# Kernel tuning notes

Hardware: AMD Instinct MI355X
Metric: run time of the kernel (lower is better)

Reference implementation:

```python
import math
import jax, jax.numpy as jnp
import numpy as np

B, S, D, H = 2, 2048, 1024, 16
DH = D // H


def setup_inputs() -> dict:
    key = jax.random.key(0)
    ks = jax.random.split(key, 6)
    scale = 1.0 / math.sqrt(D)  # xavier-ish scale for stability
    inp = {
        "query": jax.random.normal(ks[0], (B, S, D), jnp.float32),
        "mask": jax.random.randint(ks[1], (B, S, S), 0, 2) > 0,
        "Wq": jax.random.normal(ks[2], (D, D), jnp.float32) * scale,
        "bq": jnp.zeros((D,), jnp.float32),
        "Wk": jax.random.normal(ks[3], (D, D), jnp.float32) * scale,
        "bk": jnp.zeros((D,), jnp.float32),
        "Wv": jax.random.normal(ks[4], (D, D), jnp.float32) * scale,
        "bv": jnp.zeros((D,), jnp.float32),
        "Wo": jax.random.normal(ks[5], (D, D), jnp.float32) * scale,
        "bo": jnp.zeros((D,), jnp.float32),
    }
    return inp


def reference(query, mask, Wq, bq, Wk, bk, Wv, bv, Wo, bo):
    # self-attention: memory = query
    def shape(x):  # [B,S,D] -> [B,H,S,DH]
        return x.reshape(B, S, H, DH).transpose(0, 2, 1, 3)

    q = shape(query @ Wq.T + bq) / math.sqrt(DH)
    k = shape(query @ Wk.T + bk)
    v = shape(query @ Wv.T + bv)
    scores = jnp.einsum("bhqd,bhkd->bhqk", q, k)
    scores = jnp.where(mask[:, None, :, :], jnp.float32(-1e18), scores)
    attn = jax.nn.softmax(scores, axis=-1)
    # dropout is identity in eval mode
    ctx = jnp.einsum("bhqk,bhkd->bhqd", attn, v)
    ctx = ctx.transpose(0, 2, 1, 3).reshape(B, S, D)
    return ctx @ Wo.T + bo
```

## Files before the change

### kernel.cpp

```cpp
#include <hip/hip_runtime.h>

#define B_ 2
#define S_ 2048
#define D_ 1024
#define H_ 16
#define DH_ 64

typedef float f32x4 __attribute__((ext_vector_type(4)));
typedef short s16x8 __attribute__((ext_vector_type(8)));
typedef __bf16 bf16x8 __attribute__((ext_vector_type(8)));
typedef unsigned int uint;

template <typename T>
static __device__ auto mfma_sel(T a, T b, f32x4 c, int)
    -> decltype(__builtin_amdgcn_mfma_f32_16x16x32_bf16(a, b, c, 0, 0, 0)) {
  return __builtin_amdgcn_mfma_f32_16x16x32_bf16(a, b, c, 0, 0, 0);
}
template <typename T>
static __device__ f32x4 mfma_sel(T a, T b, f32x4 c, long) {
  return __builtin_amdgcn_mfma_f32_16x16x32_bf16(
      __builtin_bit_cast(bf16x8, a), __builtin_bit_cast(bf16x8, b), c, 0, 0, 0);
}
static __device__ __forceinline__ f32x4 mfma_bf16(s16x8 a, s16x8 b, f32x4 c) {
  return mfma_sel(a, b, c, 0);
}

static __device__ __forceinline__ short f2bf(float f) {
  unsigned u = __float_as_uint(f);
  u += 0x7fffu + ((u >> 16) & 1u);
  return (short)(u >> 16);
}

static __device__ __forceinline__ short f2bf_rn(float f) {
  return __builtin_bit_cast(short, (__bf16)f);
}

static __device__ __forceinline__ void async16(const short* g, short* l) {
  __builtin_amdgcn_global_load_lds(
      (const __attribute__((address_space(1))) unsigned int*)g,
      (__attribute__((address_space(3))) unsigned int*)l, 16, 0, 0);
}

__global__ void detect_mask_kernel(const uint* __restrict__ m,
                                   int* __restrict__ flag) {
  int lane = threadIdx.x;
  bool gt1 = false, notf = false;
  for (int i = 0; i < 16; ++i) {
    uint v = m[lane * 16 + i];
    if (v > 1u) gt1 = true;
    if (v != 0u && v != 0x3F800000u) notf = true;
  }
  unsigned long long b1 = __ballot(gt1);
  unsigned long long b2 = __ballot(notf);
  if (lane == 0) {
    int f;
    if (b1 == 0ull) f = 1;
    else if (b2 == 0ull) f = 2;
    else f = 0;
    *flag = f;
  }
}

__global__ __launch_bounds__(256) void build_bitmask_kernel(
    const void* __restrict__ mask, const int* __restrict__ flag,
    uint* __restrict__ bmT) {
  int w = blockIdx.x * 256 + threadIdx.x;
  int b = w >> 17;
  int rem = w & 131071;
  int q = rem >> 6;
  int kt = rem & 63;
  int mty = *flag;
  uint bits = 0;
  if (mty == 0) {
    const uint* p = (const uint*)((const unsigned char*)mask +
                                  ((size_t)b * S_ + q) * S_ + (size_t)kt * 32);
#pragma unroll
    for (int i = 0; i < 8; ++i) {
      uint v = p[i];
#pragma unroll
      for (int j = 0; j < 4; ++j)
        if ((v >> (8 * j)) & 0xffu) bits |= 1u << (i * 4 + j);
    }
  } else {
    const uint* p = (const uint*)mask + ((size_t)b * S_ + q) * S_ + kt * 32;
#pragma unroll
    for (int i = 0; i < 32; ++i)
      if (p[i]) bits |= 1u << i;
  }
  bmT[((size_t)b * (S_ / 32) + kt) * S_ + q] = bits;
}

__global__ __launch_bounds__(256) void convert_kernel(
    const float* __restrict__ q, const float* __restrict__ wq,
    const float* __restrict__ wk, const float* __restrict__ wv,
    short* __restrict__ qbf, short* __restrict__ wqkv) {
  int bid = blockIdx.x;
  int t = threadIdx.x;
  const float* src;
  short* dst;
  int rowbase, seg;
  if (bid < 2048)      { src = q;  dst = qbf;  rowbase = bid * 2;          seg = -1; }
  else if (bid < 2560) { src = wq; dst = wqkv; rowbase = (bid - 2048) * 2; seg = 0; }
  else if (bid < 3072) { src = wk; dst = wqkv; rowbase = (bid - 2560) * 2; seg = 1; }
  else                 { src = wv; dst = wqkv; rowbase = (bid - 3072) * 2; seg = 2; }
  int rl = rowbase + (t >> 7);
  int k = (t & 127) * 8;
  const float* s8 = src + (size_t)rl * 1024 + k;
  f32x4 a = *(const f32x4*)s8;
  f32x4 b = *(const f32x4*)(s8 + 4);
  s16x8 r;
  r[0] = f2bf(a[0]); r[1] = f2bf(a[1]); r[2] = f2bf(a[2]); r[3] = f2bf(a[3]);
  r[4] = f2bf(b[0]); r[5] = f2bf(b[1]); r[6] = f2bf(b[2]); r[7] = f2bf(b[3]);
  int grow = (seg < 0) ? rl : (seg * 1024 + rl);
  size_t chunk = ((size_t)(grow >> 4) * 32 + (k >> 5)) * 64 +
                 ((k >> 3) & 3) * 16 + (grow & 15);
  *(s16x8*)(dst + chunk * 8) = r;
}

__global__ __launch_bounds__(256) void convert_wo_kernel(
    const float* __restrict__ wo, short* __restrict__ wob) {
  size_t i = ((size_t)blockIdx.x * 256 + threadIdx.x) * 8;
  f32x4 a = *(const f32x4*)(wo + i);
  f32x4 b = *(const f32x4*)(wo + i + 4);
  s16x8 r;
  r[0] = f2bf(a[0]); r[1] = f2bf(a[1]); r[2] = f2bf(a[2]); r[3] = f2bf(a[3]);
  r[4] = f2bf(b[0]); r[5] = f2bf(b[1]); r[6] = f2bf(b[2]); r[7] = f2bf(b[3]);
  *(s16x8*)(wob + i) = r;
}

__global__ __launch_bounds__(256) void gemm_qkv_kernel(
    const short* __restrict__ A, const short* __restrict__ Bt,
    const float* __restrict__ bq, const float* __restrict__ bk,
    const float* __restrict__ bv, short* __restrict__ q_ws,
    short* __restrict__ KF, short* __restrict__ VF) {
  __shared__ short lds[8192];
  const int tid = threadIdx.x;
  const int lane = tid & 63;
  const int wave = tid >> 6;
  const int l16 = lane & 15;
  const int quad = lane >> 4;
  const int mb0 = blockIdx.x * 8;
  const int nb0 = blockIdx.y * 8;
  const int m0 = blockIdx.x * 128 + (wave >> 1) * 64;
  const int n0 = blockIdx.y * 128 + (wave & 1) * 64;
  const int g = tid >> 6, c = tid & 63;

  f32x4 acc[4][4];
#pragma unroll
  for (int i = 0; i < 4; ++i)
#pragma unroll
    for (int j = 0; j < 4; ++j) acc[i][j] = (f32x4){0.f, 0.f, 0.f, 0.f};

  for (int kb = 0; kb < 32; ++kb) {
    async16(A + (((size_t)(mb0 + g) * 32 + kb) * 64 + c) * 8, lds + tid * 8);
    async16(A + (((size_t)(mb0 + g + 4) * 32 + kb) * 64 + c) * 8,
            lds + 2048 + tid * 8);
    async16(Bt + (((size_t)(nb0 + g) * 32 + kb) * 64 + c) * 8,
            lds + 4096 + tid * 8);
    async16(Bt + (((size_t)(nb0 + g + 4) * 32 + kb) * 64 + c) * 8,
            lds + 6144 + tid * 8);
    __syncthreads();
    s16x8 a[4], b[4];
#pragma unroll
    for (int i = 0; i < 4; ++i)
      a[i] = *(const s16x8*)(lds + (((wave >> 1) * 4 + i) * 64 + lane) * 8);
#pragma unroll
    for (int j = 0; j < 4; ++j)
      b[j] = *(const s16x8*)(lds + 4096 + (((wave & 1) * 4 + j) * 64 + lane) * 8);
#pragma unroll
    for (int i = 0; i < 4; ++i)
#pragma unroll
      for (int j = 0; j < 4; ++j) acc[i][j] = mfma_bf16(a[i], b[j], acc[i][j]);
    __syncthreads();
  }

#pragma unroll
  for (int i = 0; i < 4; ++i) {
#pragma unroll
    for (int j = 0; j < 4; ++j) {
#pragma unroll
      for (int r = 0; r < 4; ++r) {
        int m = m0 + i * 16 + quad * 4 + r;
        int n = n0 + j * 16 + l16;
        int seg = n >> 10, nl = n & 1023;
        float bias = (seg == 0) ? bq[nl] : ((seg == 1) ? bk[nl] : bv[nl]);
        float v = acc[i][j][r] + bias;
        if (seg == 0) v *= 0.18033688011112042f;
        int bb = m >> 11, s = m & (S_ - 1);
        int hh = nl >> 6, dh = nl & 63;
        int bh = bb * H_ + hh;
        short bv16 = f2bf(v);
        if (seg == 0) {
          q_ws[((size_t)bh * S_ + s) * DH_ + dh] = bv16;
        } else if (seg == 1) {
          int kt = s >> 5, r5 = s & 31;
          int kkb = r5 >> 4, kl16 = r5 & 15;
          int kf = dh >> 5, qd = (dh >> 3) & 3, e = dh & 7;
          KF[(size_t)bh * 131072 +
             ((size_t)kt * 256 + (kkb * 2 + kf) * 64 + qd * 16 + kl16) * 8 + e] = bv16;
        } else {
          int kt = s >> 5, ko = s & 31;
          int hi = ko >> 4, qd = (ko >> 2) & 3, j4 = ko & 3;
          int nb = dh >> 4, vl16 = dh & 15, e = hi * 4 + j4;
          VF[(size_t)bh * 131072 +
             ((size_t)kt * 256 + nb * 64 + qd * 16 + vl16) * 8 + e] = bv16;
        }
      }
    }
  }
}

__global__ __launch_bounds__(512, 4) void attn_kernel(
    const short* __restrict__ Q, const short* __restrict__ KF,
    const short* __restrict__ VF, const uint* __restrict__ bmT,
    short* __restrict__ ctx_out) {
  __shared__ short lds[18432];
  const int tid = threadIdx.x;
  const int lane = tid & 63;
  const int wave = tid >> 6;
  const int qw = wave >> 1;
  const int kbt = wave & 1;
  const int l16 = lane & 15;
  const int quad = lane >> 4;
  const int xcd = blockIdx.x & 7;
  const int slot = blockIdx.x >> 3;
  const int bh = xcd * 4 + (slot >> 4);
  const int qt128 = slot & 15;
  const int b = bh >> 4;
  const int h = bh & 15;
  const int qbase = qt128 * 128 + qw * 32;

  const short* Qh = Q + (size_t)bh * S_ * DH_;
  const short* KFb = KF + (size_t)bh * 131072;
  const short* VFb = VF + (size_t)bh * 131072;
  const uint* bmb = bmT + (size_t)b * (S_ / 32) * S_;

  s16x8 qf[2][2];
#pragma unroll
  for (int qg = 0; qg < 2; ++qg)
#pragma unroll
    for (int kf = 0; kf < 2; ++kf)
      qf[qg][kf] = *(const s16x8*)(Qh + (size_t)(qbase + qg * 16 + l16) * DH_ +
                                   kf * 32 + quad * 8);

  f32x4 ctx[2][4];
#pragma unroll
  for (int qg = 0; qg < 2; ++qg)
#pragma unroll
    for (int nb = 0; nb < 4; ++nb) ctx[qg][nb] = (f32x4){0.f, 0.f, 0.f, 0.f};
  float ls[2] = {0.f, 0.f};

  async16(KFb + tid * 8, lds + tid * 8);
  async16(VFb + tid * 8, lds + 4096 + tid * 8);
  uint w0 = bmb[(size_t)kbt * S_ + qbase + l16];
  uint w1 = bmb[(size_t)kbt * S_ + qbase + 16 + l16];
  __syncthreads();

  for (int kt2 = 0; kt2 < S_ / 64; ++kt2) {
    uint wn0 = 0, wn1 = 0;
    if (kt2 < S_ / 64 - 1) {
      const int st = ((kt2 & 1) ^ 1) << 13;
      const short* kg = KFb + (size_t)(kt2 + 1) * 4096;
      const short* vg = VFb + (size_t)(kt2 + 1) * 4096;
      async16(kg + tid * 8, lds + st + tid * 8);
      async16(vg + tid * 8, lds + st + 4096 + tid * 8);
      wn0 = bmb[(size_t)(2 * (kt2 + 1) + kbt) * S_ + qbase + l16];
      wn1 = bmb[(size_t)(2 * (kt2 + 1) + kbt) * S_ + qbase + 16 + l16];
    }
    const short* kls = lds + ((kt2 & 1) << 13);
    const short* vls = kls + 4096;

    s16x8 ka[2][2];
#pragma unroll
    for (int kb = 0; kb < 2; ++kb)
#pragma unroll
      for (int kf = 0; kf < 2; ++kf)
        ka[kb][kf] =
            *(const s16x8*)(kls + kbt * 2048 + ((kb * 2 + kf) * 64 + lane) * 8);

    s16x8 pa[2];
    const uint wsh[2] = {w0 >> (quad * 4), w1 >> (quad * 4)};
#pragma unroll
    for (int qg = 0; qg < 2; ++qg) {
      f32x4 sc[2];
#pragma unroll
      for (int kb = 0; kb < 2; ++kb) {
        f32x4 t = mfma_bf16(ka[kb][0], qf[qg][0], (f32x4){0.f, 0.f, 0.f, 0.f});
        sc[kb] = mfma_bf16(ka[kb][1], qf[qg][1], t);
      }
      float sum = 0.f;
#pragma unroll
      for (int kb = 0; kb < 2; ++kb)
#pragma unroll
        for (int r = 0; r < 4; ++r) {
          int bit = (wsh[qg] >> (kb * 16 + r)) & 1;
          float p = bit ? 0.f : __builtin_amdgcn_exp2f(sc[kb][r]);
          sum += p;
          pa[qg][kb * 4 + r] = f2bf_rn(p);
        }
      ls[qg] += sum;
    }

#pragma unroll
    for (int nb = 0; nb < 4; ++nb) {
      s16x8 vb = *(const s16x8*)(vls + kbt * 2048 + (nb * 64 + lane) * 8);
#pragma unroll
      for (int qg = 0; qg < 2; ++qg)
        ctx[qg][nb] = mfma_bf16(pa[qg], vb, ctx[qg][nb]);
    }
    __syncthreads();
    w0 = wn0;
    w1 = wn1;
  }

  float* fl = (float*)lds;
  const int foff = qw * 2176;
  if (kbt) {
#pragma unroll
    for (int qg = 0; qg < 2; ++qg) {
#pragma unroll
      for (int nb = 0; nb < 4; ++nb)
#pragma unroll
        for (int r = 0; r < 4; ++r)
          fl[foff + ((qg * 4 + nb) * 4 + r) * 64 + lane] = ctx[qg][nb][r];
      fl[foff + 2048 + qg * 64 + lane] = ls[qg];
    }
  }
  __syncthreads();
  if (!kbt) {
#pragma unroll
    for (int qg = 0; qg < 2; ++qg) {
#pragma unroll
      for (int nb = 0; nb < 4; ++nb)
#pragma unroll
        for (int r = 0; r < 4; ++r)
          ctx[qg][nb][r] += fl[foff + ((qg * 4 + nb) * 4 + r) * 64 + lane];
      ls[qg] += fl[foff + 2048 + qg * 64 + lane];
      ls[qg] += __shfl_xor(ls[qg], 16);
      ls[qg] += __shfl_xor(ls[qg], 32);
    }

#pragma unroll
    for (int qg = 0; qg < 2; ++qg)
#pragma unroll
      for (int r = 0; r < 4; ++r) {
        float lr = __shfl(ls[qg], quad * 4 + r);
        float inv = 1.f / lr;
        int srow = qbase + qg * 16 + quad * 4 + r;
#pragma unroll
        for (int nb = 0; nb < 4; ++nb) {
          int col = h * DH_ + nb * 16 + l16;
          ctx_out[(size_t)(b * S_ + srow) * D_ + col] = f2bf(ctx[qg][nb][r] * inv);
        }
      }
  }
}

__global__ __launch_bounds__(256) void gemm_final_kernel(
    const short* __restrict__ A, const short* __restrict__ Bt,
    const float* __restrict__ bias, float* __restrict__ out) {
  __shared__ short lds[8192];
  const int tid = threadIdx.x;
  const int lane = tid & 63;
  const int wave = tid >> 6;
  const int l16 = lane & 15;
  const int quad = lane >> 4;
  const int m0 = blockIdx.x * 128;
  const int n0 = blockIdx.y * 128;
  const int g = tid >> 6, c = tid & 63;
  const int r15 = c & 15, qd = c >> 4;

  f32x4 acc[4][4];
#pragma unroll
  for (int i = 0; i < 4; ++i)
#pragma unroll
    for (int j = 0; j < 4; ++j) acc[i][j] = (f32x4){0.f, 0.f, 0.f, 0.f};

  for (int k0 = 0; k0 < 1024; k0 += 32) {
    async16(A + (size_t)(m0 + g * 16 + r15) * 1024 + k0 + qd * 8, lds + tid * 8);
    async16(A + (size_t)(m0 + (g + 4) * 16 + r15) * 1024 + k0 + qd * 8,
            lds + 2048 + tid * 8);
    async16(Bt + (size_t)(n0 + g * 16 + r15) * 1024 + k0 + qd * 8,
            lds + 4096 + tid * 8);
    async16(Bt + (size_t)(n0 + (g + 4) * 16 + r15) * 1024 + k0 + qd * 8,
            lds + 6144 + tid * 8);
    __syncthreads();
    s16x8 a[4], b[4];
#pragma unroll
    for (int i = 0; i < 4; ++i)
      a[i] = *(const s16x8*)(lds + (((wave >> 1) * 4 + i) * 64 + lane) * 8);
#pragma unroll
    for (int j = 0; j < 4; ++j)
      b[j] = *(const s16x8*)(lds + 4096 + (((wave & 1) * 4 + j) * 64 + lane) * 8);
#pragma unroll
    for (int i = 0; i < 4; ++i)
#pragma unroll
      for (int j = 0; j < 4; ++j) acc[i][j] = mfma_bf16(a[i], b[j], acc[i][j]);
    __syncthreads();
  }

  const int mw = m0 + (wave >> 1) * 64;
  const int nw = n0 + (wave & 1) * 64;
#pragma unroll
  for (int i = 0; i < 4; ++i)
#pragma unroll
    for (int j = 0; j < 4; ++j)
#pragma unroll
      for (int r = 0; r < 4; ++r) {
        int m = mw + i * 16 + quad * 4 + r;
        int n = nw + j * 16 + l16;
        out[(size_t)m * 1024 + n] = acc[i][j][r] + bias[n];
      }
}

extern "C" void kernel_launch(void* const* d_in, const int* in_sizes, int n_in,
                              void* d_out, int out_size, void* d_ws,
                              size_t ws_size, hipStream_t stream) {
  const float* query = (const float*)d_in[0];
  const void* mask = d_in[1];
  const float* Wq = (const float*)d_in[2];
  const float* bq = (const float*)d_in[3];
  const float* Wk = (const float*)d_in[4];
  const float* bk = (const float*)d_in[5];
  const float* Wv = (const float*)d_in[6];
  const float* bv = (const float*)d_in[7];
  const float* Wo = (const float*)d_in[8];
  const float* bo = (const float*)d_in[9];

  const size_t NE = (size_t)B_ * S_ * D_;
  short* ws_s = (short*)d_ws;
  short* q_ws = ws_s;
  short* KF = ws_s + NE;
  short* VF = ws_s + 2 * NE;
  short* ctx_ws = ws_s + 3 * NE;
  short* wo_bf = ws_s;
  short* qbf = (short*)d_out;
  short* wqkv = qbf + NE;
  uint* bmT = (uint*)(wqkv + 3145728);
  int* flag = (int*)(bmT + 262144);

  detect_mask_kernel<<<1, 64, 0, stream>>>((const uint*)mask, flag);
  build_bitmask_kernel<<<1024, 256, 0, stream>>>(mask, flag, bmT);
  convert_kernel<<<3584, 256, 0, stream>>>(query, Wq, Wk, Wv, qbf, wqkv);

  gemm_qkv_kernel<<<dim3(32, 24), 256, 0, stream>>>(qbf, wqkv, bq, bk, bv,
                                                    q_ws, KF, VF);

  attn_kernel<<<512, 512, 0, stream>>>(q_ws, KF, VF, bmT, ctx_ws);

  convert_wo_kernel<<<512, 256, 0, stream>>>(Wo, wo_bf);

  gemm_final_kernel<<<dim3(32, 8), 256, 0, stream>>>(ctx_ws, wo_bf, bo,
                                                     (float*)d_out);
}
```

Before: 237.1 us.

## Triple-buffer K/V tiles with prefetch distance two and raised MFMA priority

The attention inner loop moves from a double-buffered LDS ring to a three-slot ring, issuing async K/V loads and mask loads two tiles ahead. The loop is unrolled by three with a macro so slot offsets are constants. __syncthreads is replaced by an explicit vmcnt wait plus s_barrier, and s_setprio raises wave priority around the MFMA section. The intent is to hide global-load latency better. In exchange, LDS per block grows, which may reduce how many blocks fit per CU. The final iterations also prefetch past the end of the per-head K/V and mask data.

New measurement: 376.1 us. 58.6% more time.

```diff
diff --git a/kernel.cpp b/kernel.cpp
--- a/kernel.cpp
+++ b/kernel.cpp
@@ -214,7 +214,7 @@
     const short* __restrict__ Q, const short* __restrict__ KF,
     const short* __restrict__ VF, const uint* __restrict__ bmT,
     short* __restrict__ ctx_out) {
-  __shared__ short lds[18432];
+  __shared__ short lds[24576];
   const int tid = threadIdx.x;
   const int lane = tid & 63;
   const int wave = tid >> 6;
@@ -250,68 +250,84 @@
     for (int nb = 0; nb < 4; ++nb) ctx[qg][nb] = (f32x4){0.f, 0.f, 0.f, 0.f};
   float ls[2] = {0.f, 0.f};
 
+  uint wc0 = bmb[(size_t)kbt * S_ + qbase + l16];
+  uint wc1 = bmb[(size_t)kbt * S_ + qbase + 16 + l16];
+  uint wn0 = bmb[(size_t)(2 + kbt) * S_ + qbase + l16];
+  uint wn1 = bmb[(size_t)(2 + kbt) * S_ + qbase + 16 + l16];
+  const uint* mp = bmb + (size_t)(4 + kbt) * S_ + qbase + l16;
+
   async16(KFb + tid * 8, lds + tid * 8);
   async16(VFb + tid * 8, lds + 4096 + tid * 8);
-  uint w0 = bmb[(size_t)kbt * S_ + qbase + l16];
-  uint w1 = bmb[(size_t)kbt * S_ + qbase + 16 + l16];
+  async16(KFb + 4096 + tid * 8, lds + 8192 + tid * 8);
+  async16(VFb + 4096 + tid * 8, lds + 12288 + tid * 8);
+  const short* kg = KFb + 8192 + tid * 8;
+  const short* vg = VFb + 8192 + tid * 8;
+  asm volatile("s_waitcnt vmcnt(2)" ::: "memory");
+  __builtin_amdgcn_s_barrier();
+  __builtin_amdgcn_sched_barrier(0);
+
+  const short* kvb = lds + kbt * 2048 + lane * 8;
+
+#define ATTN_BODY(SLOT)                                                       \
+  {                                                                           \
+    uint a0 = mp[0];                                                          \
+    uint a1 = mp[16];                                                         \
+    mp += 4096;                                                               \
+    async16(kg, lds + (((SLOT) + 2) % 3) * 8192 + tid * 8);                   \
+    async16(vg, lds + (((SLOT) + 2) % 3) * 8192 + 4096 + tid * 8);            \
+    kg += 4096;                                                               \
+    vg += 4096;                                                               \
+    s16x8 ka[2][2];                                                           \
+    _Pragma("unroll") for (int kb = 0; kb < 2; ++kb)                          \
+        _Pragma("unroll") for (int kf = 0; kf < 2; ++kf)                      \
+            ka[kb][kf] = *(const s16x8*)(kvb + (SLOT) * 8192 +                \
+                                         (kb * 2 + kf) * 512);                \
+    __builtin_amdgcn_s_setprio(1);                                            \
+    s16x8 pa[2];                                                              \
+    const uint wsh0 = wc0 >> (quad * 4);                                      \
+    const uint wsh1 = wc1 >> (quad * 4);                                      \
+    _Pragma("unroll") for (int qg = 0; qg < 2; ++qg) {                        \
+      f32x4 sc[2];                                                            \
+      _Pragma("unroll") for (int kb = 0; kb < 2; ++kb) {                      \
+        f32x4 t0 = mfma_bf16(ka[kb][0], qf[qg][0], (f32x4){0.f, 0.f, 0.f, 0.f}); \
+        sc[kb] = mfma_bf16(ka[kb][1], qf[qg][1], t0);                         \
+      }                                                                       \
+      const uint wsh = qg ? wsh1 : wsh0;                                      \
+      float sum = 0.f;                                                        \
+      _Pragma("unroll") for (int kb = 0; kb < 2; ++kb)                        \
+          _Pragma("unroll") for (int r = 0; r < 4; ++r) {                     \
+        int bit = (wsh >> (kb * 16 + r)) & 1;                                 \
+        float p = bit ? 0.f : __builtin_amdgcn_exp2f(sc[kb][r]);              \
+        sum += p;                                                             \
+        pa[qg][kb * 4 + r] = f2bf_rn(p);                                      \
+      }                                                                       \
+      ls[qg] += sum;                                                          \
+    }                                                                         \
+    _Pragma("unroll") for (int nb = 0; nb < 4; ++nb) {                        \
+      s16x8 vb = *(const s16x8*)(kvb + (SLOT) * 8192 + 4096 + nb * 512);      \
+      _Pragma("unroll") for (int qg = 0; qg < 2; ++qg)                        \
+          ctx[qg][nb] = mfma_bf16(pa[qg], vb, ctx[qg][nb]);                   \
+    }                                                                         \
+    __builtin_amdgcn_s_setprio(0);                                            \
+    asm volatile("s_waitcnt vmcnt(2)" ::: "memory");                          \
+    __builtin_amdgcn_s_barrier();                                             \
+    __builtin_amdgcn_sched_barrier(0);                                        \
+    wc0 = wn0;                                                                \
+    wc1 = wn1;                                                                \
+    wn0 = a0;                                                                 \
+    wn1 = a1;                                                                 \
+  }
+
+  for (int t3 = 0; t3 < 30; t3 += 3) {
+    ATTN_BODY(0)
+    ATTN_BODY(1)
+    ATTN_BODY(2)
+  }
+  ATTN_BODY(0)
+  ATTN_BODY(1)
+#undef ATTN_BODY
+
   __syncthreads();
-
-  for (int kt2 = 0; kt2 < S_ / 64; ++kt2) {
-    uint wn0 = 0, wn1 = 0;
-    if (kt2 < S_ / 64 - 1) {
-      const int st = ((kt2 & 1) ^ 1) << 13;
-      const short* kg = KFb + (size_t)(kt2 + 1) * 4096;
-      const short* vg = VFb + (size_t)(kt2 + 1) * 4096;
-      async16(kg + tid * 8, lds + st + tid * 8);
-      async16(vg + tid * 8, lds + st + 4096 + tid * 8);
-      wn0 = bmb[(size_t)(2 * (kt2 + 1) + kbt) * S_ + qbase + l16];
-      wn1 = bmb[(size_t)(2 * (kt2 + 1) + kbt) * S_ + qbase + 16 + l16];
-    }
-    const short* kls = lds + ((kt2 & 1) << 13);
-    const short* vls = kls + 4096;
-
-    s16x8 ka[2][2];
-#pragma unroll
-    for (int kb = 0; kb < 2; ++kb)
-#pragma unroll
-      for (int kf = 0; kf < 2; ++kf)
-        ka[kb][kf] =
-            *(const s16x8*)(kls + kbt * 2048 + ((kb * 2 + kf) * 64 + lane) * 8);
-
-    s16x8 pa[2];
-    const uint wsh[2] = {w0 >> (quad * 4), w1 >> (quad * 4)};
-#pragma unroll
-    for (int qg = 0; qg < 2; ++qg) {
-      f32x4 sc[2];
-#pragma unroll
-      for (int kb = 0; kb < 2; ++kb) {
-        f32x4 t = mfma_bf16(ka[kb][0], qf[qg][0], (f32x4){0.f, 0.f, 0.f, 0.f});
-        sc[kb] = mfma_bf16(ka[kb][1], qf[qg][1], t);
-      }
-      float sum = 0.f;
-#pragma unroll
-      for (int kb = 0; kb < 2; ++kb)
-#pragma unroll
-        for (int r = 0; r < 4; ++r) {
-          int bit = (wsh[qg] >> (kb * 16 + r)) & 1;
-          float p = bit ? 0.f : __builtin_amdgcn_exp2f(sc[kb][r]);
-          sum += p;
-          pa[qg][kb * 4 + r] = f2bf_rn(p);
-        }
-      ls[qg] += sum;
-    }
-
-#pragma unroll
-    for (int nb = 0; nb < 4; ++nb) {
-      s16x8 vb = *(const s16x8*)(vls + kbt * 2048 + (nb * 64 + lane) * 8);
-#pragma unroll
-      for (int qg = 0; qg < 2; ++qg)
-        ctx[qg][nb] = mfma_bf16(pa[qg], vb, ctx[qg][nb]);
-    }
-    __syncthreads();
-    w0 = wn0;
-    w1 = wn1;
-  }
 
   float* fl = (float*)lds;
   const int foff = qw * 2176;
```
